# Performance work log

Measured on AMD Instinct MI355X. Metric: run time of the kernel, lower is better.

## Reference

```python
import jax, jax.numpy as jnp
import numpy as np

RADIUS = 0.2
K = 32  # num_neighbors


def setup_inputs() -> dict:
    key = jax.random.key(0)
    k1, k2, k3 = jax.random.split(key, 3)
    points_xyz = jax.random.uniform(k1, (2, 16384, 3), dtype=jnp.float32)
    center_xyz = jax.random.uniform(k2, (2, 2048, 3), dtype=jnp.float32)
    features = jax.random.normal(k3, (2, 64, 16384), dtype=jnp.float32)
    return {"points_xyz": points_xyz, "center_xyz": center_xyz, "features": features}


def _ball_query(center_xyz, points_xyz, k, radius):
    # squared distances (B, G, N) via ||c||^2 + ||p||^2 - 2 c.p (avoids (B,G,N,3) temp)
    c2 = jnp.sum(center_xyz * center_xyz, axis=-1)  # (B, G)
    p2 = jnp.sum(points_xyz * points_xyz, axis=-1)  # (B, N)
    cp = jnp.einsum('bgd,bnd->bgn', center_xyz, points_xyz)
    d2 = c2[:, :, None] + p2[:, None, :] - 2.0 * cp  # (B, G, N)
    n = points_xyz.shape[1]
    # key = point index if inside ball else sentinel N; first-K-in-ball == K smallest keys
    keys = jnp.where(d2 < radius * radius, jnp.arange(n, dtype=jnp.int32), n)
    neg_vals, _ = jax.lax.top_k(-keys, k)
    idx = -neg_vals  # (B, G, K) ascending point indices, sentinel n if <k found
    first = idx[..., :1]
    # pad missing slots with first found index (CUDA ball_query semantics), 0 if none
    idx = jnp.where(idx < n, idx, jnp.where(first < n, first, 0))
    return idx


def reference(points_xyz, center_xyz, features):
    idx = _ball_query(center_xyz, points_xyz, K, RADIUS)  # (B, G, K) int32
    gather = jax.vmap(lambda f, i: f[:, i])  # (C, N), (G, K) -> (C, G, K)
    grouped_xyz = gather(jnp.swapaxes(points_xyz, 1, 2), idx)  # (B, 3, G, K)
    # relative_xyz then normalize_xyz
    grouped_xyz = (grouped_xyz - jnp.swapaxes(center_xyz, 1, 2)[..., None]) / RADIUS
    grouped_features = gather(features, idx)  # (B, C, G, K)
    return grouped_xyz, grouped_features
```

## Files before the change

kernel.cpp:

```cpp
#include <hip/hip_runtime.h>
#include <hip/hip_bf16.h>

constexpr int NPTS = 16384;
constexpr int NCTR = 2048;
constexpr int NCH  = 64;
constexpr int KK   = 32;
constexpr int NB   = 2;
#define R2 0.04f

__global__ __launch_bounds__(256) void prep_kernel(
    const float* __restrict__ points,
    const float* __restrict__ feats,
    float* __restrict__ featsT,
    float4* __restrict__ packed)
{
#pragma clang fp contract(off)
    __shared__ float tile[64][65];

    if (blockIdx.x < 512) {
        const int b  = blockIdx.x >> 8;
        const int n0 = (blockIdx.x & 255) * 64;
        const int t  = threadIdx.x;
        const int nl = t & 63;
        const int q  = t >> 6;

        const float* fb = feats + (size_t)b * NCH * NPTS;
#pragma unroll
        for (int r = 0; r < 16; ++r) {
            int c = r * 4 + q;
            tile[c][nl] = fb[(size_t)c * NPTS + n0 + nl];
        }
        __syncthreads();
        float* ftb = featsT + ((size_t)b * NPTS + n0) * NCH;
#pragma unroll
        for (int r = 0; r < 16; ++r) {
            int n = r * 4 + q;
            ftb[(size_t)n * NCH + nl] = tile[nl][n];
        }
        return;
    }

    const int tid = (blockIdx.x - 512) * 256 + threadIdx.x;
#pragma unroll
    for (int s = 0; s < 4; ++s) {
        const int i = tid + s * 8192;
        const float x = points[3 * i + 0];
        const float y = points[3 * i + 1];
        const float z = points[3 * i + 2];
        const float p2 = (x * x + y * y) + z * z;
        packed[i] = make_float4(x + x, y + y, z + z, p2);
    }
}

__global__ __launch_bounds__(64, 4) void query_group(
    const float4* __restrict__ packed,
    const float* __restrict__ centers,
    const float* __restrict__ featsT,
    float* __restrict__ out_xyz,
    float* __restrict__ out_feat)
{
#pragma clang fp contract(off)
    __shared__ int   idxs[KK];
    __shared__ float sf[KK][68];

    const int lane = threadIdx.x;
    const int cg   = blockIdx.x;
    const int b    = cg >> 11;
    const int g    = cg & (NCTR - 1);

    const float4* pk = packed + (size_t)b * NPTS;
    const float* cc = centers + (size_t)cg * 3;
    const float cx = cc[0], cy = cc[1], cz = cc[2];
    const float c2 = (cx * cx + cy * cy) + cz * cz;

    float4 cur[8], nxt[8];
#pragma unroll
    for (int j = 0; j < 8; ++j) cur[j] = pk[j * 64 + lane];
    int cnt = 0;
    const unsigned long long lmask = (1ull << lane) - 1ull;
    for (int base = 0; base < NPTS; base += 512) {
        const int nbb = (base + 512 < NPTS) ? base + 512 : 0;
#pragma unroll
        for (int j = 0; j < 8; ++j) nxt[j] = pk[nbb + j * 64 + lane];

        unsigned long long m[8];
#pragma unroll
        for (int j = 0; j < 8; ++j) {
            const float4 v = cur[j];
            const float cp2 = (cx * v.x + cy * v.y) + cz * v.z;
            m[j] = __ballot((c2 + v.w) - cp2 < R2);
        }
        int run = cnt;
#pragma unroll
        for (int j = 0; j < 8; ++j) {
            if ((m[j] >> lane) & 1ull) {
                const int slot = run + __popcll(m[j] & lmask);
                if (slot < KK) idxs[slot] = base + j * 64 + lane;
            }
            run += (int)__popcll(m[j]);
        }
        cnt = run;
        if (cnt >= KK) break;
#pragma unroll
        for (int j = 0; j < 8; ++j) cur[j] = nxt[j];
    }

    const int cpd = cnt < KK ? cnt : KK;
    const int first = (cnt > 0) ? idxs[0] : 0;
    if (lane < KK) {
        const int id = (lane < cpd) ? idxs[lane] : first;
        idxs[lane] = id;
        const float4 v = pk[id];
        const float px = 0.5f * v.x, py = 0.5f * v.y, pz = 0.5f * v.z;
        const size_t ob = (((size_t)b * 3 + 0) * NCTR + g) * KK + lane;
        out_xyz[ob + (size_t)0 * NCTR * KK] = (px - cx) / 0.2f;
        out_xyz[ob + (size_t)1 * NCTR * KK] = (py - cy) / 0.2f;
        out_xyz[ob + (size_t)2 * NCTR * KK] = (pz - cz) / 0.2f;
    }

    const int li = lane & 15, r = lane >> 4;
    const float* ftb = featsT + (size_t)b * NPTS * NCH;
#pragma unroll
    for (int i = 0; i < 8; ++i) {
        const int k = i * 4 + r;
        const float4 v = *((const float4*)(ftb + (size_t)idxs[k] * NCH) + li);
        *(float4*)&sf[k][4 * li] = v;
    }

    const int kq = lane & 3, c0 = lane >> 2;
    const size_t ob = ((size_t)b * NCH * NCTR + g) * KK;
#pragma unroll
    for (int h = 0; h < 2; ++h) {
#pragma unroll
        for (int p = 0; p < 4; ++p) {
            const int c = c0 + 16 * p;
            const int k = 16 * h + 4 * kq;
            float4 w;
            w.x = sf[k + 0][c];
            w.y = sf[k + 1][c];
            w.z = sf[k + 2][c];
            w.w = sf[k + 3][c];
            *(float4*)(out_feat + ob + (size_t)c * NCTR * KK + k) = w;
        }
    }
}

__global__ __launch_bounds__(256) void ballquery_group(
    const float* __restrict__ points, const float* __restrict__ centers,
    const float* __restrict__ feats, float* __restrict__ out_xyz,
    float* __restrict__ out_feat)
{
#pragma clang fp contract(off)
    __shared__ int   s_idx[4][KK];
    __shared__ float s_f[4][KK][65];
    const int wave = threadIdx.x >> 6, lane = threadIdx.x & 63;
    const int cg = blockIdx.x * 4 + wave;
    const int b = cg >> 11, g = cg & (NCTR - 1);
    const float* pb = points + (size_t)b * NPTS * 3;
    const float* cc = centers + (size_t)cg * 3;
    const float cx = cc[0], cy = cc[1], cz = cc[2];
    const float c2 = (cx * cx + cy * cy) + cz * cz;
    int* idxs = s_idx[wave];
    int cnt = 0;
    for (int base = 0; base < NPTS; base += 64) {
        const int i = base + lane;
        const float px = pb[i * 3 + 0], py = pb[i * 3 + 1], pz = pb[i * 3 + 2];
        const float p2 = (px * px + py * py) + pz * pz;
        const float cp = (cx * px + cy * py) + cz * pz;
        const float d2 = (c2 + p2) - 2.0f * cp;
        const bool hit = d2 < R2;
        const unsigned long long m = __ballot(hit);
        if (hit) {
            const int slot = cnt + __popcll(m & ((1ull << lane) - 1ull));
            if (slot < KK) idxs[slot] = i;
        }
        cnt += (int)__popcll(m);
        if (cnt >= KK) break;
    }
    __syncthreads();
    const int cpd = cnt < KK ? cnt : KK;
    const int first = (cnt > 0) ? idxs[0] : 0;
    if (lane < KK) idxs[lane] = (lane < cpd) ? idxs[lane] : first;
    __syncthreads();
    if (lane < KK) {
        const int id = idxs[lane];
        const float px = pb[id * 3 + 0], py = pb[id * 3 + 1], pz = pb[id * 3 + 2];
        const size_t ob = (((size_t)b * 3 + 0) * NCTR + g) * KK + lane;
        out_xyz[ob + (size_t)0 * NCTR * KK] = (px - cx) / 0.2f;
        out_xyz[ob + (size_t)1 * NCTR * KK] = (py - cy) / 0.2f;
        out_xyz[ob + (size_t)2 * NCTR * KK] = (pz - cz) / 0.2f;
    }
    float (*sf)[65] = s_f[wave];
    const float* fb = feats + (size_t)b * NCH * NPTS;
    for (int k = 0; k < KK; ++k) {
        const int id = idxs[k];
        sf[k][lane] = fb[(size_t)lane * NPTS + id];
    }
    __syncthreads();
    const int k = lane & 31, ch = lane >> 5;
    const size_t ob = ((size_t)b * NCH * NCTR + g) * KK;
#pragma unroll
    for (int cc2 = 0; cc2 < 32; ++cc2) {
        const int c = cc2 * 2 + ch;
        out_feat[ob + (size_t)c * NCTR * KK + k] = sf[k][c];
    }
}

extern "C" void kernel_launch(void* const* d_in, const int* in_sizes, int n_in,
                              void* d_out, int out_size, void* d_ws, size_t ws_size,
                              hipStream_t stream) {
    const float* points  = (const float*)d_in[0];
    const float* centers = (const float*)d_in[1];
    const float* feats   = (const float*)d_in[2];

    float* out      = (float*)d_out;
    float* out_xyz  = out;
    float* out_feat = out + (size_t)NB * 3 * NCTR * KK;

    const size_t ftBytes = (size_t)NB * NPTS * NCH * sizeof(float);
    const size_t pkBytes = (size_t)NB * NPTS * 4 * sizeof(float);

    if (ws_size >= ftBytes + pkBytes) {
        float*  featsT = (float*)d_ws;
        float4* packed = (float4*)((char*)d_ws + ftBytes);
        prep_kernel<<<544, 256, 0, stream>>>(points, feats, featsT, packed);
        query_group<<<NB * NCTR, 64, 0, stream>>>(
            packed, centers, featsT, out_xyz, out_feat);
    } else {
        ballquery_group<<<(NB * NCTR) / 4, 256, 0, stream>>>(
            points, centers, feats, out_xyz, out_feat);
    }
}
```

Baseline: 86.40 us.

## Split ball-query point scan across four waves per center and merge results

```diff
diff --git a/kernel.cpp b/kernel.cpp
--- a/kernel.cpp
+++ b/kernel.cpp
@@ -52,7 +52,7 @@
     }
 }
 
-__global__ __launch_bounds__(64, 4) void query_group(
+__global__ __launch_bounds__(256, 4) void query_group(
     const float4* __restrict__ packed,
     const float* __restrict__ centers,
     const float* __restrict__ featsT,
@@ -60,10 +60,13 @@
     float* __restrict__ out_feat)
 {
 #pragma clang fp contract(off)
+    __shared__ int   lidx[4][KK];
+    __shared__ int   lcnt[4];
     __shared__ int   idxs[KK];
     __shared__ float sf[KK][68];
 
-    const int lane = threadIdx.x;
+    const int wave = threadIdx.x >> 6;
+    const int lane = threadIdx.x & 63;
     const int cg   = blockIdx.x;
     const int b    = cg >> 11;
     const int g    = cg & (NCTR - 1);
@@ -73,15 +76,17 @@
     const float cx = cc[0], cy = cc[1], cz = cc[2];
     const float c2 = (cx * cx + cy * cy) + cz * cz;
 
+    const int qb = wave * 4096 + lane;
     float4 cur[8], nxt[8];
 #pragma unroll
-    for (int j = 0; j < 8; ++j) cur[j] = pk[j * 64 + lane];
+    for (int j = 0; j < 8; ++j) cur[j] = pk[qb + j * 64];
     int cnt = 0;
     const unsigned long long lmask = (1ull << lane) - 1ull;
-    for (int base = 0; base < NPTS; base += 512) {
-        const int nbb = (base + 512 < NPTS) ? base + 512 : 0;
-#pragma unroll
-        for (int j = 0; j < 8; ++j) nxt[j] = pk[nbb + j * 64 + lane];
+    int* lp = lidx[wave];
+    for (int c = 0; c < 8; ++c) {
+        const int nc = (c < 7) ? c + 1 : 0;
+#pragma unroll
+        for (int j = 0; j < 8; ++j) nxt[j] = pk[qb + nc * 512 + j * 64];
 
         unsigned long long m[8];
 #pragma unroll
@@ -91,11 +96,12 @@
             m[j] = __ballot((c2 + v.w) - cp2 < R2);
         }
         int run = cnt;
+        const int base = wave * 4096 + c * 512;
 #pragma unroll
         for (int j = 0; j < 8; ++j) {
             if ((m[j] >> lane) & 1ull) {
                 const int slot = run + __popcll(m[j] & lmask);
-                if (slot < KK) idxs[slot] = base + j * 64 + lane;
+                if (slot < KK) lp[slot] = base + j * 64 + lane;
             }
             run += (int)__popcll(m[j]);
         }
@@ -104,44 +110,63 @@
 #pragma unroll
         for (int j = 0; j < 8; ++j) cur[j] = nxt[j];
     }
-
-    const int cpd = cnt < KK ? cnt : KK;
-    const int first = (cnt > 0) ? idxs[0] : 0;
-    if (lane < KK) {
-        const int id = (lane < cpd) ? idxs[lane] : first;
-        idxs[lane] = id;
+    if (lane == 0) lcnt[wave] = cnt < KK ? cnt : KK;
+    __syncthreads();
+
+    const int t = threadIdx.x;
+    const int n0 = lcnt[0], n01 = n0 + lcnt[1], n012 = n01 + lcnt[2];
+    const int total = n012 + lcnt[3];
+    const int cpd = total < KK ? total : KK;
+    if (t < KK) {
+        int first;
+        if (n0 > 0)        first = lidx[0][0];
+        else if (n01 > 0)  first = lidx[1][0];
+        else if (n012 > 0) first = lidx[2][0];
+        else if (total > 0) first = lidx[3][0];
+        else               first = 0;
+        int id;
+        if (t < cpd) {
+            int w, off;
+            if (t < n0)        { w = 0; off = t; }
+            else if (t < n01)  { w = 1; off = t - n0; }
+            else if (t < n012) { w = 2; off = t - n01; }
+            else               { w = 3; off = t - n012; }
+            id = lidx[w][off];
+        } else {
+            id = first;
+        }
+        idxs[t] = id;
         const float4 v = pk[id];
         const float px = 0.5f * v.x, py = 0.5f * v.y, pz = 0.5f * v.z;
-        const size_t ob = (((size_t)b * 3 + 0) * NCTR + g) * KK + lane;
+        const size_t ob = (((size_t)b * 3 + 0) * NCTR + g) * KK + t;
         out_xyz[ob + (size_t)0 * NCTR * KK] = (px - cx) / 0.2f;
         out_xyz[ob + (size_t)1 * NCTR * KK] = (py - cy) / 0.2f;
         out_xyz[ob + (size_t)2 * NCTR * KK] = (pz - cz) / 0.2f;
     }
+    __syncthreads();
 
     const int li = lane & 15, r = lane >> 4;
     const float* ftb = featsT + (size_t)b * NPTS * NCH;
 #pragma unroll
-    for (int i = 0; i < 8; ++i) {
-        const int k = i * 4 + r;
+    for (int i = 0; i < 2; ++i) {
+        const int k = wave * 8 + i * 4 + r;
         const float4 v = *((const float4*)(ftb + (size_t)idxs[k] * NCH) + li);
         *(float4*)&sf[k][4 * li] = v;
     }
-
-    const int kq = lane & 3, c0 = lane >> 2;
+    __syncthreads();
+
+    const int kq = t & 7;
+    const int c0 = t >> 3;
     const size_t ob = ((size_t)b * NCH * NCTR + g) * KK;
 #pragma unroll
-    for (int h = 0; h < 2; ++h) {
-#pragma unroll
-        for (int p = 0; p < 4; ++p) {
-            const int c = c0 + 16 * p;
-            const int k = 16 * h + 4 * kq;
-            float4 w;
-            w.x = sf[k + 0][c];
-            w.y = sf[k + 1][c];
-            w.z = sf[k + 2][c];
-            w.w = sf[k + 3][c];
-            *(float4*)(out_feat + ob + (size_t)c * NCTR * KK + k) = w;
-        }
+    for (int p = 0; p < 2; ++p) {
+        const int c = c0 + 32 * p;
+        float4 w;
+        w.x = sf[4 * kq + 0][c];
+        w.y = sf[4 * kq + 1][c];
+        w.z = sf[4 * kq + 2][c];
+        w.w = sf[4 * kq + 3][c];
+        *(float4*)(out_feat + ob + (size_t)c * NCTR * KK + 4 * kq) = w;
     }
 }
 
@@ -224,7 +249,7 @@
         float*  featsT = (float*)d_ws;
         float4* packed = (float4*)((char*)d_ws + ftBytes);
         prep_kernel<<<544, 256, 0, stream>>>(points, feats, featsT, packed);
-        query_group<<<NB * NCTR, 64, 0, stream>>>(
+        query_group<<<NB * NCTR, 256, 0, stream>>>(
             packed, centers, featsT, out_xyz, out_feat);
     } else {
         ballquery_group<<<(NB * NCTR) / 4, 256, 0, stream>>>(
```

After: 98.31 us. 13.8% more time.

## Split ball query into per-chunk count pass and parallel chunk selection

Applied to the files above, without the earlier changes.

```diff
diff --git a/kernel.cpp b/kernel.cpp
--- a/kernel.cpp
+++ b/kernel.cpp
@@ -6,41 +6,15 @@
 constexpr int NCH  = 64;
 constexpr int KK   = 32;
 constexpr int NB   = 2;
+constexpr int NCHK = 32;
 #define R2 0.04f
 
-__global__ __launch_bounds__(256) void prep_kernel(
+__global__ __launch_bounds__(256) void pack_kernel(
     const float* __restrict__ points,
-    const float* __restrict__ feats,
-    float* __restrict__ featsT,
     float4* __restrict__ packed)
 {
 #pragma clang fp contract(off)
-    __shared__ float tile[64][65];
-
-    if (blockIdx.x < 512) {
-        const int b  = blockIdx.x >> 8;
-        const int n0 = (blockIdx.x & 255) * 64;
-        const int t  = threadIdx.x;
-        const int nl = t & 63;
-        const int q  = t >> 6;
-
-        const float* fb = feats + (size_t)b * NCH * NPTS;
-#pragma unroll
-        for (int r = 0; r < 16; ++r) {
-            int c = r * 4 + q;
-            tile[c][nl] = fb[(size_t)c * NPTS + n0 + nl];
-        }
-        __syncthreads();
-        float* ftb = featsT + ((size_t)b * NPTS + n0) * NCH;
-#pragma unroll
-        for (int r = 0; r < 16; ++r) {
-            int n = r * 4 + q;
-            ftb[(size_t)n * NCH + nl] = tile[nl][n];
-        }
-        return;
-    }
-
-    const int tid = (blockIdx.x - 512) * 256 + threadIdx.x;
+    const int tid = blockIdx.x * 256 + threadIdx.x;
 #pragma unroll
     for (int s = 0; s < 4; ++s) {
         const int i = tid + s * 8192;
@@ -52,45 +26,92 @@
     }
 }
 
-__global__ __launch_bounds__(64, 4) void query_group(
+__global__ __launch_bounds__(256) void count_kernel(
     const float4* __restrict__ packed,
     const float* __restrict__ centers,
-    const float* __restrict__ featsT,
+    unsigned short* __restrict__ cnts)
+{
+#pragma clang fp contract(off)
+    const int wave = threadIdx.x >> 6, lane = threadIdx.x & 63;
+    const int W     = blockIdx.x * 4 + wave;
+    const int chunk = W & 31;
+    const int cgrp  = W >> 5;
+    const int c     = cgrp * 64 + lane;
+    const int b     = c >> 11;
+
+    const float* cc = centers + (size_t)c * 3;
+    const float cx = cc[0], cy = cc[1], cz = cc[2];
+    const float c2 = (cx * cx + cy * cy) + cz * cz;
+
+    const float4* pk = packed + (size_t)b * NPTS + chunk * 512;
+    int cnt0 = 0, cnt1 = 0;
+    for (int j = 0; j < 512; j += 8) {
+        float4 p[8];
+#pragma unroll
+        for (int u = 0; u < 8; ++u) p[u] = pk[j + u];
+#pragma unroll
+        for (int u = 0; u < 8; ++u) {
+            const float cp2 = (cx * p[u].x + cy * p[u].y) + cz * p[u].z;
+            const float d2 = (c2 + p[u].w) - cp2;
+            if (u & 1) cnt1 += (d2 < R2); else cnt0 += (d2 < R2);
+        }
+    }
+    cnts[(size_t)chunk * 4096 + c] = (unsigned short)(cnt0 + cnt1);
+}
+
+__global__ __launch_bounds__(256) void select_group(
+    const float4* __restrict__ packed,
+    const float* __restrict__ centers,
+    const float* __restrict__ feats,
+    const unsigned short* __restrict__ cnts,
     float* __restrict__ out_xyz,
     float* __restrict__ out_feat)
 {
 #pragma clang fp contract(off)
-    __shared__ int   idxs[KK];
-    __shared__ float sf[KK][68];
-
-    const int lane = threadIdx.x;
-    const int cg   = blockIdx.x;
-    const int b    = cg >> 11;
-    const int g    = cg & (NCTR - 1);
+    __shared__ int scnt[NCHK];
+    __shared__ int sexcl[NCHK];
+    __shared__ int sCH, sTot;
+    __shared__ int idxs[KK];
+
+    const int t = threadIdx.x, wave = t >> 6, lane = t & 63;
+    const int cg = blockIdx.x;
+    const int b  = cg >> 11;
+    const int g  = cg & (NCTR - 1);
 
     const float4* pk = packed + (size_t)b * NPTS;
     const float* cc = centers + (size_t)cg * 3;
     const float cx = cc[0], cy = cc[1], cz = cc[2];
     const float c2 = (cx * cx + cy * cy) + cz * cz;
 
-    float4 cur[8], nxt[8];
-#pragma unroll
-    for (int j = 0; j < 8; ++j) cur[j] = pk[j * 64 + lane];
-    int cnt = 0;
+    if (t < NCHK) scnt[t] = cnts[(size_t)t * 4096 + cg];
+    __syncthreads();
+    if (t == 0) {
+        int run = 0, CH = NCHK - 1;
+        for (int q = 0; q < NCHK; ++q) {
+            sexcl[q] = run;
+            run += scnt[q];
+            if (CH == NCHK - 1 && run >= KK) CH = q;
+        }
+        sCH = CH; sTot = run;
+    }
+    __syncthreads();
+
+    const int CH = sCH;
     const unsigned long long lmask = (1ull << lane) - 1ull;
-    for (int base = 0; base < NPTS; base += 512) {
-        const int nbb = (base + 512 < NPTS) ? base + 512 : 0;
-#pragma unroll
-        for (int j = 0; j < 8; ++j) nxt[j] = pk[nbb + j * 64 + lane];
-
+    for (int q = wave; q <= CH; q += 4) {
+        const int excl = sexcl[q];
+        if (excl >= KK) continue;
+        const int base = q * 512;
+        float4 v[8];
+#pragma unroll
+        for (int j = 0; j < 8; ++j) v[j] = pk[base + j * 64 + lane];
         unsigned long long m[8];
 #pragma unroll
         for (int j = 0; j < 8; ++j) {
-            const float4 v = cur[j];
-            const float cp2 = (cx * v.x + cy * v.y) + cz * v.z;
-            m[j] = __ballot((c2 + v.w) - cp2 < R2);
-        }
-        int run = cnt;
+            const float cp2 = (cx * v[j].x + cy * v[j].y) + cz * v[j].z;
+            m[j] = __ballot((c2 + v[j].w) - cp2 < R2);
+        }
+        int run = excl;
 #pragma unroll
         for (int j = 0; j < 8; ++j) {
             if ((m[j] >> lane) & 1ull) {
@@ -99,49 +120,37 @@
             }
             run += (int)__popcll(m[j]);
         }
-        cnt = run;
-        if (cnt >= KK) break;
-#pragma unroll
-        for (int j = 0; j < 8; ++j) cur[j] = nxt[j];
-    }
-
-    const int cpd = cnt < KK ? cnt : KK;
-    const int first = (cnt > 0) ? idxs[0] : 0;
-    if (lane < KK) {
-        const int id = (lane < cpd) ? idxs[lane] : first;
-        idxs[lane] = id;
-        const float4 v = pk[id];
+    }
+    __syncthreads();
+
+    const int total = sTot;
+    const int cpd = total < KK ? total : KK;
+    int myid = 0;
+    if (t < KK) {
+        const int first = (total > 0) ? idxs[0] : 0;
+        myid = (t < cpd) ? idxs[t] : first;
+    }
+    __syncthreads();
+    if (t < KK) {
+        idxs[t] = myid;
+        const float4 v = pk[myid];
         const float px = 0.5f * v.x, py = 0.5f * v.y, pz = 0.5f * v.z;
-        const size_t ob = (((size_t)b * 3 + 0) * NCTR + g) * KK + lane;
+        const size_t ob = (((size_t)b * 3 + 0) * NCTR + g) * KK + t;
         out_xyz[ob + (size_t)0 * NCTR * KK] = (px - cx) / 0.2f;
         out_xyz[ob + (size_t)1 * NCTR * KK] = (py - cy) / 0.2f;
         out_xyz[ob + (size_t)2 * NCTR * KK] = (pz - cz) / 0.2f;
     }
-
-    const int li = lane & 15, r = lane >> 4;
-    const float* ftb = featsT + (size_t)b * NPTS * NCH;
+    __syncthreads();
+
+    const int k  = t & 31;
+    const int c0 = t >> 5;
+    const int id = idxs[k];
+    const float* fb = feats + (size_t)b * NCH * NPTS;
+    float* ofb = out_feat + ((size_t)b * NCH * NCTR + g) * KK + k;
 #pragma unroll
     for (int i = 0; i < 8; ++i) {
-        const int k = i * 4 + r;
-        const float4 v = *((const float4*)(ftb + (size_t)idxs[k] * NCH) + li);
-        *(float4*)&sf[k][4 * li] = v;
-    }
-
-    const int kq = lane & 3, c0 = lane >> 2;
-    const size_t ob = ((size_t)b * NCH * NCTR + g) * KK;
-#pragma unroll
-    for (int h = 0; h < 2; ++h) {
-#pragma unroll
-        for (int p = 0; p < 4; ++p) {
-            const int c = c0 + 16 * p;
-            const int k = 16 * h + 4 * kq;
-            float4 w;
-            w.x = sf[k + 0][c];
-            w.y = sf[k + 1][c];
-            w.z = sf[k + 2][c];
-            w.w = sf[k + 3][c];
-            *(float4*)(out_feat + ob + (size_t)c * NCTR * KK + k) = w;
-        }
+        const int c = c0 + 8 * i;
+        ofb[(size_t)c * NCTR * KK] = fb[(size_t)c * NPTS + id];
     }
 }
 
@@ -217,15 +226,16 @@
     float* out_xyz  = out;
     float* out_feat = out + (size_t)NB * 3 * NCTR * KK;
 
-    const size_t ftBytes = (size_t)NB * NPTS * NCH * sizeof(float);
     const size_t pkBytes = (size_t)NB * NPTS * 4 * sizeof(float);
-
-    if (ws_size >= ftBytes + pkBytes) {
-        float*  featsT = (float*)d_ws;
-        float4* packed = (float4*)((char*)d_ws + ftBytes);
-        prep_kernel<<<544, 256, 0, stream>>>(points, feats, featsT, packed);
-        query_group<<<NB * NCTR, 64, 0, stream>>>(
-            packed, centers, featsT, out_xyz, out_feat);
+    const size_t cntBytes = (size_t)NCHK * NB * NCTR * sizeof(unsigned short);
+
+    if (ws_size >= pkBytes + cntBytes) {
+        float4* packed = (float4*)d_ws;
+        unsigned short* cnts = (unsigned short*)((char*)d_ws + pkBytes);
+        pack_kernel<<<32, 256, 0, stream>>>(points, packed);
+        count_kernel<<<512, 256, 0, stream>>>(packed, centers, cnts);
+        select_group<<<NB * NCTR, 256, 0, stream>>>(
+            packed, centers, feats, cnts, out_xyz, out_feat);
     } else {
         ballquery_group<<<(NB * NCTR) / 4, 256, 0, stream>>>(
             points, centers, feats, out_xyz, out_feat);
```

New measurement: 134.2 us. 1.55x slower.
